# Kernel optimization log

Measured on AMD Instinct MI355X. Metric: run time of the kernel, lower is better.

Reference implementation:

```python
import jax, jax.numpy as jnp
import numpy as np

B, C, H, W = 4, 256, 64, 64
HID = max(C // 8, 64)  # = 64


def setup_inputs() -> dict:
    key = jax.random.key(0)
    ks = jax.random.split(key, 8)
    s_in = 1.0 / np.sqrt(C)
    return {
        "x1": jax.random.normal(ks[0], (B, C, H, W), dtype=jnp.float32),
        "x2": jax.random.normal(ks[1], (B, C, H, W), dtype=jnp.float32),
        "Wq": jax.random.normal(ks[2], (HID, C), dtype=jnp.float32) * s_in,
        "bq": jnp.zeros((HID,), dtype=jnp.float32),
        "Wk": jax.random.normal(ks[3], (HID, C), dtype=jnp.float32) * s_in,
        "bk": jnp.zeros((HID,), dtype=jnp.float32),
        "Wv": jax.random.normal(ks[4], (C, C), dtype=jnp.float32) * s_in,
        "bv": jnp.zeros((C,), dtype=jnp.float32),
        "gamma": jnp.ones((1,), dtype=jnp.float32) * 0.5,  # nonzero so attention path matters
    }


def _conv1x1(x, Wt, b):
    # 1x1 conv == per-pixel GEMM: (O,C) x (B,C,H,W) -> (B,O,H,W)
    return jnp.einsum("oc,bchw->bohw", Wt, x) + b[None, :, None, None]


def _cross_attend(xq, xkv, Wq, bq, Wk, bk, Wv, bv, gamma):
    b, c, h, w = xq.shape
    n = h * w
    q = _conv1x1(xq, Wq, bq).reshape(b, -1, n)    # (B, hid, N)
    k = _conv1x1(xkv, Wk, bk).reshape(b, -1, n)   # (B, hid, N)
    v = _conv1x1(xkv, Wv, bv).reshape(b, c, n)    # (B, C, N)
    # attn[b,n,m] = softmax_m( q[:, :, n] . k[:, :, m] )
    attn = jax.nn.softmax(jnp.einsum("bhn,bhm->bnm", q, k), axis=-1)
    out = jnp.einsum("bcm,bnm->bcn", v, attn).reshape(b, c, h, w)
    return xq + gamma[0] * out


def reference(x1, x2, Wq, bq, Wk, bk, Wv, bv, gamma):
    x1_att = _cross_attend(x1, x2, Wq, bq, Wk, bk, Wv, bv, gamma)
    x2_att = _cross_attend(x2, x1, Wq, bq, Wk, bk, Wv, bv, gamma)
    return (x1_att, x2_att)
```

## Files before the change

kernel.cpp:

```cpp
#include <hip/hip_runtime.h>
#include <hip/hip_bf16.h>

#define NPIX 4096
#define CCH  256
#define HID  64
#define BAT  4
#define XSTR 264
#define PTS  136
#define RTHR 8.0f


using f32x4 = __attribute__((ext_vector_type(4))) float;
using h16x8 = __attribute__((ext_vector_type(8))) _Float16;
using u16x4 = __attribute__((ext_vector_type(4))) unsigned short;

#define L2E 1.44269504088896340736f

__device__ __forceinline__ unsigned short f2h(float f) {
    _Float16 h = (_Float16)f;
    return __builtin_bit_cast(unsigned short, h);
}
__device__ __forceinline__ h16x8 ldg_fragh(const unsigned short* p) {
    uint4 v = *reinterpret_cast<const uint4*>(p);
    return __builtin_bit_cast(h16x8, v);
}
__device__ __forceinline__ h16x8 lds_fragh(const unsigned short* p) {
    return *reinterpret_cast<const h16x8*>(p);
}
__device__ __forceinline__ unsigned int pk2h(float a, float b) {
    auto t = __builtin_amdgcn_cvt_pkrtz(a, b);
    return __builtin_bit_cast(unsigned int, t);
}
__device__ __forceinline__ float sel4(float a0, float a1, float a2, float a3, int q) {
    float x = (q & 1) ? a1 : a0;
    float y = (q & 1) ? a3 : a2;
    return (q & 2) ? y : x;
}

__global__ __launch_bounds__(256, 1) void wcvt_kernel(
    const float* __restrict__ Wq, const float* __restrict__ Wk,
    const float* __restrict__ Wv, unsigned short* __restrict__ Wg)
{
    int tid = blockIdx.x * 256 + threadIdx.x;
    int tile = tid >> 6, lane = tid & 63;
    int r = (tile >> 3) * 16 + (lane & 15);
    int c = (tile & 7) * 32 + (lane >> 4) * 8;
    const float* src; float sc;
    if (r < 64)       { src = Wq + r * CCH + c;        sc = L2E; }
    else if (r < 128) { src = Wk + (r - 64) * CCH + c; sc = 1.0f; }
    else              { src = Wv + (r - 128) * CCH + c; sc = 1.0f; }
    float4 a = *reinterpret_cast<const float4*>(src);
    float4 b4 = *reinterpret_cast<const float4*>(src + 4);
    uint4 out;
    out.x = pk2h(a.x * sc, a.y * sc);
    out.y = pk2h(a.z * sc, a.w * sc);
    out.z = pk2h(b4.x * sc, b4.y * sc);
    out.w = pk2h(b4.z * sc, b4.w * sc);
    *reinterpret_cast<uint4*>(Wg + tile * 512 + lane * 8) = out;
}

__global__ __launch_bounds__(256, 2) void proj_kernel(
    const float* __restrict__ x1, const float* __restrict__ x2,
    const unsigned short* __restrict__ Wg,
    const float* __restrict__ bq, const float* __restrict__ bk,
    const float* __restrict__ bv,
    unsigned short* __restrict__ Qf, unsigned short* __restrict__ Kf,
    unsigned short* __restrict__ Vt)
{
    __shared__ unsigned short xs[32][XSTR];

    const int Lb = blockIdx.x;
    const int sb = Lb & 7;
    const int tile = Lb >> 3;
    const int s = sb >> 2, b = sb & 3;
    const float* x = s ? x2 : x1;
    const int n0 = tile * 32;
    const int t = threadIdx.x;
    const int lane = t & 63;
    const int w = __builtin_amdgcn_readfirstlane(t >> 6);
    const int quad = lane >> 4, lq = lane & 15;

    {
        const int n = t & 31;
        const int g = t >> 5;
        const float* xb = x + (size_t)(b * CCH) * NPIX + n0;
        #pragma unroll
        for (int i = 0; i < 8; ++i) {
            int c0 = g * 4 + i * 32;
            u16x4 hv;
            #pragma unroll
            for (int j = 0; j < 4; ++j)
                hv[j] = f2h(xb[(size_t)(c0 + j) * NPIX + n]);
            *reinterpret_cast<u16x4*>(&xs[n][c0]) = hv;
        }
    }
    __syncthreads();

    h16x8 xf[2][8];
    #pragma unroll
    for (int nt = 0; nt < 2; ++nt)
        #pragma unroll
        for (int ks = 0; ks < 8; ++ks)
            xf[nt][ks] = lds_fragh(&xs[nt * 16 + lq][ks * 32 + quad * 8]);

    unsigned short* Qb = Qf + (size_t)(s * BAT + b) * (NPIX * HID);
    unsigned short* Kb = Kf + (size_t)(s * BAT + b) * (NPIX * HID);
    unsigned short* Vb = Vt + (size_t)(s * BAT + b) * ((size_t)CCH * NPIX);

    h16x8 wf[2][8];
    {
        const unsigned short* wp = Wg + (size_t)(w * 6 * 8) * 512 + lane * 8;
        #pragma unroll
        for (int ks = 0; ks < 8; ++ks) wf[0][ks] = ldg_fragh(wp + ks * 512);
    }

    #pragma unroll
    for (int hloop = 0; hloop < 6; ++hloop) {
        const int cur = hloop & 1;
        const int idx = w * 6 + hloop;
        const int kind = idx < 4 ? 0 : (idx < 8 ? 1 : 2);

        if (hloop < 5) {
            const unsigned short* wp = Wg + (size_t)((idx + 1) * 8) * 512 + lane * 8;
            #pragma unroll
            for (int ks = 0; ks < 8; ++ks) wf[cur ^ 1][ks] = ldg_fragh(wp + ks * 512);
        }

        if (kind == 2) {
            const int cbase = (idx - 8) * 16;
            const float bbv = bv[cbase + lq];
            #pragma unroll
            for (int nt = 0; nt < 2; ++nt) {
                f32x4 acc = (f32x4){0.f, 0.f, 0.f, 0.f};
                #pragma unroll
                for (int ks = 0; ks < 8; ++ks)
                    acc = __builtin_amdgcn_mfma_f32_16x16x32_f16(xf[nt][ks], wf[cur][ks], acc, 0, 0, 0);
                u16x4 pk;
                #pragma unroll
                for (int reg = 0; reg < 4; ++reg) pk[reg] = f2h(acc[reg] + bbv);
                size_t off = (size_t)((idx - 8) * 128 + (n0 >> 5)) * 512
                           + (nt * 2 + (quad >> 1)) * 128 + lq * 8 + (quad & 1) * 4;
                *reinterpret_cast<unsigned long long*>(Vb + off) =
                    __builtin_bit_cast(unsigned long long, pk);
            }
        } else {
            unsigned short* dq = (kind ? Kb : Qb);
            const float* bias = (kind ? bk : bq);
            const float scl = kind ? 1.0f : L2E;
            const int hb16 = kind ? (idx - 4) : idx;
            float bb4[4];
            #pragma unroll
            for (int reg = 0; reg < 4; ++reg)
                bb4[reg] = bias[hb16 * 16 + quad * 4 + reg] * scl;
            #pragma unroll
            for (int nt = 0; nt < 2; ++nt) {
                f32x4 acc = (f32x4){0.f, 0.f, 0.f, 0.f};
                #pragma unroll
                for (int ks = 0; ks < 8; ++ks)
                    acc = __builtin_amdgcn_mfma_f32_16x16x32_f16(wf[cur][ks], xf[nt][ks], acc, 0, 0, 0);
                u16x4 pk;
                #pragma unroll
                for (int reg = 0; reg < 4; ++reg) pk[reg] = f2h(acc[reg] + bb4[reg]);
                size_t off = (size_t)((n0 >> 4) + nt) * 1024 + (hb16 >> 1) * 512
                           + ((hb16 & 1) * 2 + (quad >> 1)) * 128 + lq * 8 + (quad & 1) * 4;
                *reinterpret_cast<unsigned long long*>(dq + off) =
                    __builtin_bit_cast(unsigned long long, pk);
            }
        }
    }
}

__global__ __launch_bounds__(256, 2) void attn_kernel(
    const float* __restrict__ x1, const float* __restrict__ x2,
    const unsigned short* __restrict__ Qf, const unsigned short* __restrict__ Kf,
    const unsigned short* __restrict__ Vt,
    const float* __restrict__ gamma, float* __restrict__ out)
{
    __shared__ unsigned short PT[2][64 * PTS];
    __shared__ float Lsh[4][64];
    __shared__ float Tsh[4][64];

    const int Lb = blockIdx.x;
    const int g = Lb & 7;
    const int ntile = Lb >> 3;
    const int d = g >> 2, b = g & 3;
    const int db = d * BAT + b;
    const int s = d, r = 1 - d;
    const int n0 = ntile * 64;

    const int t = threadIdx.x;
    const int lane = t & 63;
    const int w = __builtin_amdgcn_readfirstlane(t >> 6);
    const int quad = lane >> 4, lq = lane & 15;

    const unsigned short* Qb = Qf + (size_t)(s * BAT + b) * (NPIX * HID);
    const unsigned short* Kb = Kf + (size_t)(r * BAT + b) * (NPIX * HID);
    const unsigned short* Vb = Vt + (size_t)(r * BAT + b) * ((size_t)CCH * NPIX);

    h16x8 qf[4][2];
    #pragma unroll
    for (int nt = 0; nt < 4; ++nt)
        #pragma unroll
        for (int ks = 0; ks < 2; ++ks)
            qf[nt][ks] = ldg_fragh(Qb + (size_t)((((n0 >> 4) + nt) * 2) + ks) * 512 + lane * 8);

    f32x4 Oacc[4][4];
    #pragma unroll
    for (int rt = 0; rt < 4; ++rt)
        #pragma unroll
        for (int ct = 0; ct < 4; ++ct)
            Oacc[rt][ct] = (f32x4){0.f, 0.f, 0.f, 0.f};

    float Li[4] = {0.f, 0.f, 0.f, 0.f};
    float Mv[4] = {0.f, 0.f, 0.f, 0.f};

    h16x8 kf[2][2];
    #pragma unroll
    for (int mt = 0; mt < 2; ++mt)
        #pragma unroll
        for (int ks = 0; ks < 2; ++ks)
            kf[mt][ks] = ldg_fragh(Kb + (size_t)((w * 2 + mt) * 2 + ks) * 512 + lane * 8);

    h16x8 vf[4][4];
    #pragma unroll
    for (int ks = 0; ks < 4; ++ks)
        #pragma unroll
        for (int rt = 0; rt < 4; ++rt)
            vf[ks][rt] = ldg_fragh(Vb + (size_t)((w * 4 + rt) * 128 + ks) * 512 + lane * 8);

    for (int it = 0; it < 32; ++it) {
        const int buf = it & 1;

        f32x4 Sacc[2][4];
        #pragma unroll
        for (int mt = 0; mt < 2; ++mt)
            #pragma unroll
            for (int nt = 0; nt < 4; ++nt)
                Sacc[mt][nt] = (f32x4){-Mv[nt], -Mv[nt], -Mv[nt], -Mv[nt]};
        #pragma unroll
        for (int mt = 0; mt < 2; ++mt)
            #pragma unroll
            for (int ks = 0; ks < 2; ++ks)
                #pragma unroll
                for (int nt = 0; nt < 4; ++nt)
                    Sacc[mt][nt] = __builtin_amdgcn_mfma_f32_16x16x32_f16(
                        kf[mt][ks], qf[nt][ks], Sacc[mt][nt], 0, 0, 0);

        const int itk = (it < 31) ? it + 1 : 31;
        #pragma unroll
        for (int mt = 0; mt < 2; ++mt)
            #pragma unroll
            for (int ks = 0; ks < 2; ++ks)
                kf[mt][ks] = ldg_fragh(Kb + (size_t)((itk * 8 + w * 2 + mt) * 2 + ks) * 512
                                          + lane * 8);

        float trel[4];
        #pragma unroll
        for (int nt = 0; nt < 4; ++nt) {
            float ta = fmaxf(fmaxf(Sacc[0][nt][0], Sacc[0][nt][1]),
                             fmaxf(Sacc[0][nt][2], Sacc[0][nt][3]));
            float tb = fmaxf(fmaxf(Sacc[1][nt][0], Sacc[1][nt][1]),
                             fmaxf(Sacc[1][nt][2], Sacc[1][nt][3]));
            float tm = fmaxf(ta, tb);
            tm = fmaxf(tm, __shfl_xor(tm, 16));
            tm = fmaxf(tm, __shfl_xor(tm, 32));
            trel[nt] = tm;
        }
        Tsh[w][quad * 16 + lq] = sel4(trel[0], trel[1], trel[2], trel[3], quad);
        __syncthreads();

        float bm[4];
        #pragma unroll
        for (int nt = 0; nt < 4; ++nt) {
            int i = nt * 16 + lq;
            bm[nt] = fmaxf(fmaxf(Tsh[0][i], Tsh[1][i]),
                           fmaxf(Tsh[2][i], Tsh[3][i]));
        }
        if (__any((bm[0] > RTHR) || (bm[1] > RTHR) ||
                  (bm[2] > RTHR) || (bm[3] > RTHR))) {
            #pragma unroll
            for (int nt = 0; nt < 4; ++nt) {
                float dlt = fmaxf(bm[nt], 0.f);
                float sc = __builtin_amdgcn_exp2f(-dlt);
                Mv[nt] += dlt;
                Li[nt] *= sc;
                #pragma unroll
                for (int mt = 0; mt < 2; ++mt)
                    #pragma unroll
                    for (int rg = 0; rg < 4; ++rg)
                        Sacc[mt][nt][rg] -= dlt;
                #pragma unroll
                for (int rt = 0; rt < 4; ++rt)
                    #pragma unroll
                    for (int rg = 0; rg < 4; ++rg)
                        Oacc[rt][nt][rg] *= sc;
            }
        }

        #pragma unroll
        for (int mt = 0; mt < 2; ++mt)
            #pragma unroll
            for (int nt = 0; nt < 4; ++nt) {
                float p0 = __builtin_amdgcn_exp2f(Sacc[mt][nt][0]);
                float p1 = __builtin_amdgcn_exp2f(Sacc[mt][nt][1]);
                float p2 = __builtin_amdgcn_exp2f(Sacc[mt][nt][2]);
                float p3 = __builtin_amdgcn_exp2f(Sacc[mt][nt][3]);
                Li[nt] += (p0 + p1) + (p2 + p3);
                uint2 pk2;
                pk2.x = pk2h(p0, p1);
                pk2.y = pk2h(p2, p3);
                *reinterpret_cast<uint2*>(
                    &PT[buf][(nt * 16 + lq) * PTS + w * 32 + mt * 16 + quad * 4]) = pk2;
            }
        __syncthreads();

        #pragma unroll
        for (int ks = 0; ks < 4; ++ks) {
            h16x8 pf[4];
            #pragma unroll
            for (int ct = 0; ct < 4; ++ct)
                pf[ct] = lds_fragh(&PT[buf][(ct * 16 + lq) * PTS + ks * 32 + quad * 8]);
            #pragma unroll
            for (int rt = 0; rt < 4; ++rt)
                #pragma unroll
                for (int ct = 0; ct < 4; ++ct)
                    Oacc[rt][ct] = __builtin_amdgcn_mfma_f32_16x16x32_f16(
                        vf[ks][rt], pf[ct], Oacc[rt][ct], 0, 0, 0);
        }

        const int itv = (it < 31) ? it + 1 : 31;
        #pragma unroll
        for (int ks = 0; ks < 4; ++ks)
            #pragma unroll
            for (int rt = 0; rt < 4; ++rt)
                vf[ks][rt] = ldg_fragh(Vb + (size_t)((w * 4 + rt) * 128 + itv * 4 + ks) * 512
                                          + lane * 8);
    }

    #pragma unroll
    for (int nt = 0; nt < 4; ++nt) {
        Li[nt] += __shfl_xor(Li[nt], 16);
        Li[nt] += __shfl_xor(Li[nt], 32);
    }
    Lsh[w][quad * 16 + lq] = sel4(Li[0], Li[1], Li[2], Li[3], quad);
    __syncthreads();

    float inv[4];
    #pragma unroll
    for (int nt = 0; nt < 4; ++nt) {
        int i = nt * 16 + lq;
        inv[nt] = 1.0f / ((Lsh[0][i] + Lsh[1][i]) + (Lsh[2][i] + Lsh[3][i]));
    }

    const float* xq = d ? x2 : x1;
    const float gm = gamma[0];

    #pragma unroll
    for (int rt = 0; rt < 4; ++rt)
        #pragma unroll
        for (int ct = 0; ct < 4; ++ct)
            #pragma unroll
            for (int rg = 0; rg < 4; ++rg) {
                int c = w * 64 + rt * 16 + quad * 4 + rg;
                int nn = n0 + ct * 16 + lq;
                size_t src = (size_t)(b * CCH + c) * NPIX + nn;
                size_t dst = (size_t)(db * CCH + c) * NPIX + nn;
                out[dst] = xq[src] + gm * Oacc[rt][ct][rg] * inv[ct];
            }
}

extern "C" void kernel_launch(void* const* d_in, const int* in_sizes, int n_in,
                              void* d_out, int out_size, void* d_ws, size_t ws_size,
                              hipStream_t stream) {
    (void)in_sizes; (void)n_in; (void)out_size; (void)ws_size;
    const float* x1 = (const float*)d_in[0];
    const float* x2 = (const float*)d_in[1];
    const float* Wq = (const float*)d_in[2];
    const float* bq = (const float*)d_in[3];
    const float* Wk = (const float*)d_in[4];
    const float* bk = (const float*)d_in[5];
    const float* Wv = (const float*)d_in[6];
    const float* bv = (const float*)d_in[7];
    const float* gm = (const float*)d_in[8];
    float* out = (float*)d_out;

    unsigned short* ws = (unsigned short*)d_ws;
    unsigned short* Qf = ws;
    unsigned short* Kf = Qf + (size_t)2097152;
    unsigned short* Vt = Kf + (size_t)2097152;
    unsigned short* Wg = Vt + (size_t)8388608;

    wcvt_kernel<<<dim3(48), dim3(256), 0, stream>>>(Wq, Wk, Wv, Wg);
    proj_kernel<<<dim3(1024), dim3(256), 0, stream>>>(
        x1, x2, Wg, bq, bk, bv, Qf, Kf, Vt);
    attn_kernel<<<dim3(512), dim3(256), 0, stream>>>(
        x1, x2, Qf, Kf, Vt, gm, out);
}
```

Before: 193.8 us.

## Split attention block across eight waves and re-layout P tile in LDS

The attention kernel goes from 4 to 8 waves per block. Each wave now handles 16 key rows for scores and 32 output channels, which roughly halves the per-wave accumulator and V-fragment registers so more waves can be resident. The P tile in LDS moves to an MFMA-fragment-native layout, so each lane reads its B operand with one contiguous 16-byte load instead of strided rows. V fragments are now double-buffered per k-step and prefetched one step ahead. In exchange there are more barrier participants and 8-way max/sum reductions through shared memory, and the global loads of K and V are issued as smaller pieces.

```diff
diff --git a/kernel.cpp b/kernel.cpp
--- a/kernel.cpp
+++ b/kernel.cpp
@@ -6,7 +6,6 @@
 #define HID  64
 #define BAT  4
 #define XSTR 264
-#define PTS  136
 #define RTHR 8.0f
 
 
@@ -170,15 +169,15 @@
     }
 }
 
-__global__ __launch_bounds__(256, 2) void attn_kernel(
+__global__ __launch_bounds__(512, 4) void attn_kernel(
     const float* __restrict__ x1, const float* __restrict__ x2,
     const unsigned short* __restrict__ Qf, const unsigned short* __restrict__ Kf,
     const unsigned short* __restrict__ Vt,
     const float* __restrict__ gamma, float* __restrict__ out)
 {
-    __shared__ unsigned short PT[2][64 * PTS];
-    __shared__ float Lsh[4][64];
-    __shared__ float Tsh[4][64];
+    __shared__ unsigned short PT[2][16 * 512];
+    __shared__ float Lsh[8][64];
+    __shared__ float Tsh[8][64];
 
     const int Lb = blockIdx.x;
     const int g = Lb & 7;
@@ -204,9 +203,9 @@
         for (int ks = 0; ks < 2; ++ks)
             qf[nt][ks] = ldg_fragh(Qb + (size_t)((((n0 >> 4) + nt) * 2) + ks) * 512 + lane * 8);
 
-    f32x4 Oacc[4][4];
-    #pragma unroll
-    for (int rt = 0; rt < 4; ++rt)
+    f32x4 Oacc[2][4];
+    #pragma unroll
+    for (int rt = 0; rt < 2; ++rt)
         #pragma unroll
         for (int ct = 0; ct < 4; ++ct)
             Oacc[rt][ct] = (f32x4){0.f, 0.f, 0.f, 0.f};
@@ -214,54 +213,44 @@
     float Li[4] = {0.f, 0.f, 0.f, 0.f};
     float Mv[4] = {0.f, 0.f, 0.f, 0.f};
 
-    h16x8 kf[2][2];
-    #pragma unroll
-    for (int mt = 0; mt < 2; ++mt)
-        #pragma unroll
-        for (int ks = 0; ks < 2; ++ks)
-            kf[mt][ks] = ldg_fragh(Kb + (size_t)((w * 2 + mt) * 2 + ks) * 512 + lane * 8);
-
-    h16x8 vf[4][4];
-    #pragma unroll
-    for (int ks = 0; ks < 4; ++ks)
-        #pragma unroll
-        for (int rt = 0; rt < 4; ++rt)
-            vf[ks][rt] = ldg_fragh(Vb + (size_t)((w * 4 + rt) * 128 + ks) * 512 + lane * 8);
+    h16x8 kf[2];
+    #pragma unroll
+    for (int ks = 0; ks < 2; ++ks)
+        kf[ks] = ldg_fragh(Kb + (size_t)(w * 2 + ks) * 512 + lane * 8);
+
+    h16x8 vf[2][2];
+    #pragma unroll
+    for (int rt = 0; rt < 2; ++rt)
+        vf[0][rt] = ldg_fragh(Vb + (size_t)((w * 2 + rt) * 128) * 512 + lane * 8);
+
+    const int koct = (w & 1) * 2 + (quad >> 1);
+    const int pwoff = koct * 128 + lq * 8 + (quad & 1) * 4;
+    const int pktile = (w >> 1);
 
     for (int it = 0; it < 32; ++it) {
         const int buf = it & 1;
 
-        f32x4 Sacc[2][4];
-        #pragma unroll
-        for (int mt = 0; mt < 2; ++mt)
+        f32x4 Sacc[4];
+        #pragma unroll
+        for (int nt = 0; nt < 4; ++nt)
+            Sacc[nt] = (f32x4){-Mv[nt], -Mv[nt], -Mv[nt], -Mv[nt]};
+        #pragma unroll
+        for (int ks = 0; ks < 2; ++ks)
             #pragma unroll
             for (int nt = 0; nt < 4; ++nt)
-                Sacc[mt][nt] = (f32x4){-Mv[nt], -Mv[nt], -Mv[nt], -Mv[nt]};
-        #pragma unroll
-        for (int mt = 0; mt < 2; ++mt)
-            #pragma unroll
-            for (int ks = 0; ks < 2; ++ks)
-                #pragma unroll
-                for (int nt = 0; nt < 4; ++nt)
-                    Sacc[mt][nt] = __builtin_amdgcn_mfma_f32_16x16x32_f16(
-                        kf[mt][ks], qf[nt][ks], Sacc[mt][nt], 0, 0, 0);
+                Sacc[nt] = __builtin_amdgcn_mfma_f32_16x16x32_f16(
+                    kf[ks], qf[nt][ks], Sacc[nt], 0, 0, 0);
 
         const int itk = (it < 31) ? it + 1 : 31;
         #pragma unroll
-        for (int mt = 0; mt < 2; ++mt)
-            #pragma unroll
-            for (int ks = 0; ks < 2; ++ks)
-                kf[mt][ks] = ldg_fragh(Kb + (size_t)((itk * 8 + w * 2 + mt) * 2 + ks) * 512
-                                          + lane * 8);
+        for (int ks = 0; ks < 2; ++ks)
+            kf[ks] = ldg_fragh(Kb + (size_t)((itk * 8 + w) * 2 + ks) * 512 + lane * 8);
 
         float trel[4];
         #pragma unroll
         for (int nt = 0; nt < 4; ++nt) {
-            float ta = fmaxf(fmaxf(Sacc[0][nt][0], Sacc[0][nt][1]),
-                             fmaxf(Sacc[0][nt][2], Sacc[0][nt][3]));
-            float tb = fmaxf(fmaxf(Sacc[1][nt][0], Sacc[1][nt][1]),
-                             fmaxf(Sacc[1][nt][2], Sacc[1][nt][3]));
-            float tm = fmaxf(ta, tb);
+            float tm = fmaxf(fmaxf(Sacc[nt][0], Sacc[nt][1]),
+                             fmaxf(Sacc[nt][2], Sacc[nt][3]));
             tm = fmaxf(tm, __shfl_xor(tm, 16));
             tm = fmaxf(tm, __shfl_xor(tm, 32));
             trel[nt] = tm;
@@ -273,8 +262,11 @@
         #pragma unroll
         for (int nt = 0; nt < 4; ++nt) {
             int i = nt * 16 + lq;
-            bm[nt] = fmaxf(fmaxf(Tsh[0][i], Tsh[1][i]),
-                           fmaxf(Tsh[2][i], Tsh[3][i]));
+            float m01 = fmaxf(Tsh[0][i], Tsh[1][i]);
+            float m23 = fmaxf(Tsh[2][i], Tsh[3][i]);
+            float m45 = fmaxf(Tsh[4][i], Tsh[5][i]);
+            float m67 = fmaxf(Tsh[6][i], Tsh[7][i]);
+            bm[nt] = fmaxf(fmaxf(m01, m23), fmaxf(m45, m67));
         }
         if (__any((bm[0] > RTHR) || (bm[1] > RTHR) ||
                   (bm[2] > RTHR) || (bm[3] > RTHR))) {
@@ -285,12 +277,10 @@
                 Mv[nt] += dlt;
                 Li[nt] *= sc;
                 #pragma unroll
-                for (int mt = 0; mt < 2; ++mt)
-                    #pragma unroll
-                    for (int rg = 0; rg < 4; ++rg)
-                        Sacc[mt][nt][rg] -= dlt;
-                #pragma unroll
-                for (int rt = 0; rt < 4; ++rt)
+                for (int rg = 0; rg < 4; ++rg)
+                    Sacc[nt][rg] -= dlt;
+                #pragma unroll
+                for (int rt = 0; rt < 2; ++rt)
                     #pragma unroll
                     for (int rg = 0; rg < 4; ++rg)
                         Oacc[rt][nt][rg] *= sc;
@@ -298,43 +288,40 @@
         }
 
         #pragma unroll
-        for (int mt = 0; mt < 2; ++mt)
-            #pragma unroll
-            for (int nt = 0; nt < 4; ++nt) {
-                float p0 = __builtin_amdgcn_exp2f(Sacc[mt][nt][0]);
-                float p1 = __builtin_amdgcn_exp2f(Sacc[mt][nt][1]);
-                float p2 = __builtin_amdgcn_exp2f(Sacc[mt][nt][2]);
-                float p3 = __builtin_amdgcn_exp2f(Sacc[mt][nt][3]);
-                Li[nt] += (p0 + p1) + (p2 + p3);
-                uint2 pk2;
-                pk2.x = pk2h(p0, p1);
-                pk2.y = pk2h(p2, p3);
-                *reinterpret_cast<uint2*>(
-                    &PT[buf][(nt * 16 + lq) * PTS + w * 32 + mt * 16 + quad * 4]) = pk2;
-            }
+        for (int nt = 0; nt < 4; ++nt) {
+            float p0 = __builtin_amdgcn_exp2f(Sacc[nt][0]);
+            float p1 = __builtin_amdgcn_exp2f(Sacc[nt][1]);
+            float p2 = __builtin_amdgcn_exp2f(Sacc[nt][2]);
+            float p3 = __builtin_amdgcn_exp2f(Sacc[nt][3]);
+            Li[nt] += (p0 + p1) + (p2 + p3);
+            uint2 pk2;
+            pk2.x = pk2h(p0, p1);
+            pk2.y = pk2h(p2, p3);
+            *reinterpret_cast<uint2*>(
+                &PT[buf][(nt * 4 + pktile) * 512 + pwoff]) = pk2;
+        }
         __syncthreads();
 
         #pragma unroll
         for (int ks = 0; ks < 4; ++ks) {
+            const int kk = it * 4 + ks;
+            const int nk = (kk < 127) ? kk + 1 : 127;
+            #pragma unroll
+            for (int rt = 0; rt < 2; ++rt)
+                vf[(ks + 1) & 1][rt] =
+                    ldg_fragh(Vb + (size_t)((w * 2 + rt) * 128 + nk) * 512 + lane * 8);
+
             h16x8 pf[4];
             #pragma unroll
             for (int ct = 0; ct < 4; ++ct)
-                pf[ct] = lds_fragh(&PT[buf][(ct * 16 + lq) * PTS + ks * 32 + quad * 8]);
-            #pragma unroll
-            for (int rt = 0; rt < 4; ++rt)
+                pf[ct] = lds_fragh(&PT[buf][(ct * 4 + ks) * 512 + lane * 8]);
+            #pragma unroll
+            for (int rt = 0; rt < 2; ++rt)
                 #pragma unroll
                 for (int ct = 0; ct < 4; ++ct)
                     Oacc[rt][ct] = __builtin_amdgcn_mfma_f32_16x16x32_f16(
-                        vf[ks][rt], pf[ct], Oacc[rt][ct], 0, 0, 0);
-        }
-
-        const int itv = (it < 31) ? it + 1 : 31;
-        #pragma unroll
-        for (int ks = 0; ks < 4; ++ks)
-            #pragma unroll
-            for (int rt = 0; rt < 4; ++rt)
-                vf[ks][rt] = ldg_fragh(Vb + (size_t)((w * 4 + rt) * 128 + itv * 4 + ks) * 512
-                                          + lane * 8);
+                        vf[ks & 1][rt], pf[ct], Oacc[rt][ct], 0, 0, 0);
+        }
     }
 
     #pragma unroll
@@ -349,19 +336,23 @@
     #pragma unroll
     for (int nt = 0; nt < 4; ++nt) {
         int i = nt * 16 + lq;
-        inv[nt] = 1.0f / ((Lsh[0][i] + Lsh[1][i]) + (Lsh[2][i] + Lsh[3][i]));
+        float s01 = Lsh[0][i] + Lsh[1][i];
+        float s23 = Lsh[2][i] + Lsh[3][i];
+        float s45 = Lsh[4][i] + Lsh[5][i];
+        float s67 = Lsh[6][i] + Lsh[7][i];
+        inv[nt] = 1.0f / ((s01 + s23) + (s45 + s67));
     }
 
     const float* xq = d ? x2 : x1;
     const float gm = gamma[0];
 
     #pragma unroll
-    for (int rt = 0; rt < 4; ++rt)
+    for (int rt = 0; rt < 2; ++rt)
         #pragma unroll
         for (int ct = 0; ct < 4; ++ct)
             #pragma unroll
             for (int rg = 0; rg < 4; ++rg) {
-                int c = w * 64 + rt * 16 + quad * 4 + rg;
+                int c = (w * 2 + rt) * 16 + quad * 4 + rg;
                 int nn = n0 + ct * 16 + lq;
                 size_t src = (size_t)(b * CCH + c) * NPIX + nn;
                 size_t dst = (size_t)(db * CCH + c) * NPIX + nn;
@@ -393,6 +384,6 @@
     wcvt_kernel<<<dim3(48), dim3(256), 0, stream>>>(Wq, Wk, Wv, Wg);
     proj_kernel<<<dim3(1024), dim3(256), 0, stream>>>(
         x1, x2, Wg, bq, bk, bv, Qf, Kf, Vt);
-    attn_kernel<<<dim3(512), dim3(256), 0, stream>>>(
+    attn_kernel<<<dim3(512), dim3(512), 0, stream>>>(
         x1, x2, Qf, Kf, Vt, gm, out);
 }
```

Result: slower. 217.2 us (+12.1%).

## Defer half of PV MFMAs into next iteration to overlap softmax reduction

Applied to the files above, without the earlier changes.

Splits the P·V MFMA step in the attention loop. The first two k-slices run right after P is written. The last two are deferred to the next iteration, where they run before the running-max rescale check, and a drain step after the loop finishes them. The aim is to hide the LDS and sync latency of the row-max reduction behind matrix work and to spread out the V fragment loads. It also drops proj_kernel's launch bounds from 2 to 1 blocks per CU, allowing more registers at the cost of occupancy.

```diff
diff --git a/kernel.cpp b/kernel.cpp
--- a/kernel.cpp
+++ b/kernel.cpp
@@ -59,7 +59,7 @@
     *reinterpret_cast<uint4*>(Wg + tile * 512 + lane * 8) = out;
 }
 
-__global__ __launch_bounds__(256, 2) void proj_kernel(
+__global__ __launch_bounds__(256, 1) void proj_kernel(
     const float* __restrict__ x1, const float* __restrict__ x2,
     const unsigned short* __restrict__ Wg,
     const float* __restrict__ bq, const float* __restrict__ bk,
@@ -276,6 +276,30 @@
             bm[nt] = fmaxf(fmaxf(Tsh[0][i], Tsh[1][i]),
                            fmaxf(Tsh[2][i], Tsh[3][i]));
         }
+
+        if (it > 0) {
+            const int pbuf = buf ^ 1;
+            #pragma unroll
+            for (int ks = 2; ks < 4; ++ks) {
+                h16x8 pf[4];
+                #pragma unroll
+                for (int ct = 0; ct < 4; ++ct)
+                    pf[ct] = lds_fragh(&PT[pbuf][(ct * 16 + lq) * PTS + ks * 32 + quad * 8]);
+                #pragma unroll
+                for (int rt = 0; rt < 4; ++rt)
+                    #pragma unroll
+                    for (int ct = 0; ct < 4; ++ct)
+                        Oacc[rt][ct] = __builtin_amdgcn_mfma_f32_16x16x32_f16(
+                            vf[ks][rt], pf[ct], Oacc[rt][ct], 0, 0, 0);
+            }
+            #pragma unroll
+            for (int ks = 2; ks < 4; ++ks)
+                #pragma unroll
+                for (int rt = 0; rt < 4; ++rt)
+                    vf[ks][rt] = ldg_fragh(Vb + (size_t)((w * 4 + rt) * 128 + it * 4 + ks) * 512
+                                              + lane * 8);
+        }
+
         if (__any((bm[0] > RTHR) || (bm[1] > RTHR) ||
                   (bm[2] > RTHR) || (bm[3] > RTHR))) {
             #pragma unroll
@@ -315,7 +339,7 @@
         __syncthreads();
 
         #pragma unroll
-        for (int ks = 0; ks < 4; ++ks) {
+        for (int ks = 0; ks < 2; ++ks) {
             h16x8 pf[4];
             #pragma unroll
             for (int ct = 0; ct < 4; ++ct)
@@ -330,11 +354,25 @@
 
         const int itv = (it < 31) ? it + 1 : 31;
         #pragma unroll
-        for (int ks = 0; ks < 4; ++ks)
+        for (int ks = 0; ks < 2; ++ks)
             #pragma unroll
             for (int rt = 0; rt < 4; ++rt)
                 vf[ks][rt] = ldg_fragh(Vb + (size_t)((w * 4 + rt) * 128 + itv * 4 + ks) * 512
                                           + lane * 8);
+    }
+
+    #pragma unroll
+    for (int ks = 2; ks < 4; ++ks) {
+        h16x8 pf[4];
+        #pragma unroll
+        for (int ct = 0; ct < 4; ++ct)
+            pf[ct] = lds_fragh(&PT[1][(ct * 16 + lq) * PTS + ks * 32 + quad * 8]);
+        #pragma unroll
+        for (int rt = 0; rt < 4; ++rt)
+            #pragma unroll
+            for (int ct = 0; ct < 4; ++ct)
+                Oacc[rt][ct] = __builtin_amdgcn_mfma_f32_16x16x32_f16(
+                    vf[ks][rt], pf[ct], Oacc[rt][ct], 0, 0, 0);
     }
 
     #pragma unroll
```

Result: slower. 202.5 us (+4.5%).
